# Optimization experiments

Measured on AMD Instinct MI355X. Metric: run time of the kernel, lower is better.

Reference implementation:

```python
import jax, jax.numpy as jnp
import numpy as np


def setup_inputs() -> dict:
    key = jax.random.key(0)
    k1, k2 = jax.random.split(key)
    n = 12000
    dataset = jax.random.normal(k1, (n,), dtype=jnp.float32)
    weights = jax.random.uniform(k2, (n,), dtype=jnp.float32)
    return {"dataset": dataset, "weights": weights}


def reference(dataset, weights):
    # normalize weights (update_weights)
    w = weights / jnp.sum(weights)
    neff = jnp.sum(w) ** 2 / jnp.sum(w ** 2)
    # Silverman's factor (torch.std is unbiased -> ddof=1; torch.quantile is linear interp)
    std_dev = jnp.std(dataset, ddof=1)
    iqr = jnp.quantile(dataset, 0.75) - jnp.quantile(dataset, 0.25)
    sigma_hat = jnp.minimum(std_dev, iqr / 1.34)
    h = 0.9 * sigma_hat * neff ** (-0.2)
    inv_norm = 1.0 / (h * jnp.sqrt(2.0 * jnp.pi))
    # pairwise Gaussian kernel matrix: [n, n]
    diff = (dataset[:, None] - dataset[None, :]) / h
    kernel = jnp.exp(-0.5 * diff * diff) * inv_norm
    pdf = kernel @ w  # [n]
    return jnp.log(pdf + 1e-10)
```

## Files before the change

### kernel.cpp

```cpp
#include <hip/hip_runtime.h>
#include <math.h>


#define BLK 256
#define NB 2048
#define NPART 12
#define CUT 4.0f

#if defined(__has_builtin)
#if __has_builtin(__builtin_amdgcn_exp2f)
#define EXP2(x) __builtin_amdgcn_exp2f(x)
#endif
#endif
#ifndef EXP2
#define EXP2(x) exp2f(x)
#endif

__global__ __launch_bounds__(1024) void kM(const float* __restrict__ d,
                                           const float* __restrict__ w,
                                           float4* __restrict__ statP,
                                           float2* __restrict__ mmP,
                                           int n) {
    __shared__ float4 sstat[16];
    __shared__ float2 smm[16];
    const int t = threadIdx.x, lane = t & 63, wid = t >> 6;
    const int i = blockIdx.x * 1024 + t;
    const bool ok = (i < n);
    float dv = ok ? d[i] : 0.f;
    float wv = ok ? w[i] : 0.f;
    float mn = ok ? dv : __int_as_float(0x7f800000);
    float mx = ok ? dv : __int_as_float(0xff800000);
    float s1 = wv, s2 = wv * wv, sd = dv, sd2 = dv * dv;
    for (int off = 32; off > 0; off >>= 1) {
        s1 += __shfl_down(s1, off); s2 += __shfl_down(s2, off);
        sd += __shfl_down(sd, off); sd2 += __shfl_down(sd2, off);
        mn = fminf(mn, __shfl_down(mn, off));
        mx = fmaxf(mx, __shfl_down(mx, off));
    }
    if (lane == 0) { sstat[wid] = make_float4(s1, s2, sd, sd2); smm[wid] = make_float2(mn, mx); }
    __syncthreads();
    if (t == 0) {
        float4 a = sstat[0]; float2 m = smm[0];
        for (int q = 1; q < 16; ++q) {
            float4 b = sstat[q];
            a.x += b.x; a.y += b.y; a.z += b.z; a.w += b.w;
            m.x = fminf(m.x, smm[q].x); m.y = fmaxf(m.y, smm[q].y);
        }
        statP[blockIdx.x] = a;
        mmP[blockIdx.x] = m;
    }
}

__global__ __launch_bounds__(1024) void kA(const float* __restrict__ d,
                                           const float* __restrict__ w,
                                           const float2* __restrict__ mmP,
                                           int* __restrict__ partH,
                                           float* __restrict__ partW,
                                           float* __restrict__ partWE,
                                           int n) {
    __shared__ int   hl[NB];
    __shared__ float wl[NB];
    __shared__ float wel[NB];
    const int t = threadIdx.x, blk = blockIdx.x;

    hl[t] = 0; hl[t + 1024] = 0;
    wl[t] = 0.f; wl[t + 1024] = 0.f;
    wel[t] = 0.f; wel[t + 1024] = 0.f;

    float lo = __int_as_float(0x7f800000), hi = __int_as_float(0xff800000);
    #pragma unroll
    for (int p = 0; p < NPART; ++p) {
        float2 m = mmP[p];
        lo = fminf(lo, m.x); hi = fmaxf(hi, m.y);
    }
    const float range = hi - lo;
    const float scale = (range > 0.f) ? (float)NB / range : 0.f;
    __syncthreads();

    const int i = blk * 1024 + t;
    if (i < n) {
        float dv = d[i], wv = w[i];
        int b = (int)((dv - lo) * scale);
        b = b < NB ? b : NB - 1;
        atomicAdd(&hl[b], 1);
        atomicAdd(&wl[b], wv);
        atomicAdd(&wel[b], wv * dv);
    }
    __syncthreads();

    partH [blk * NB + t] = hl[t];  partH [blk * NB + t + 1024] = hl[t + 1024];
    partW [blk * NB + t] = wl[t];  partW [blk * NB + t + 1024] = wl[t + 1024];
    partWE[blk * NB + t] = wel[t]; partWE[blk * NB + t + 1024] = wel[t + 1024];
}

__global__ __launch_bounds__(1024) void kB(const float4* __restrict__ statP,
                                           const float2* __restrict__ mmP,
                                           const int* __restrict__ partH,
                                           const float* __restrict__ partW,
                                           const float* __restrict__ partWE,
                                           float* __restrict__ params,
                                           float2* __restrict__ sb,
                                           int n) {
    __shared__ int cum[NB];
    __shared__ float sW[NB];
    __shared__ float sWE[NB];
    __shared__ int wtot[17];
    __shared__ float qv[4];
    __shared__ int tbin[4], tprev[4];
    __shared__ float spar[8];
    const int t = threadIdx.x, lane = t & 63, wid = t >> 6;
    const int b0 = t, b1 = t + 1024;

    int h0 = 0, h1 = 0;
    float W0 = 0.f, W1 = 0.f, E0 = 0.f, E1 = 0.f;
    #pragma unroll
    for (int p = 0; p < NPART; ++p) {
        h0 += partH[p * NB + b0];  h1 += partH[p * NB + b1];
        W0 += partW[p * NB + b0];  W1 += partW[p * NB + b1];
        E0 += partWE[p * NB + b0]; E1 += partWE[p * NB + b1];
    }
    sW[b0] = W0; sW[b1] = W1; sWE[b0] = E0; sWE[b1] = E1;

    int v = h0;
    for (int off = 1; off < 64; off <<= 1) {
        int u = __shfl_up(v, off);
        if (lane >= off) v += u;
    }
    if (lane == 63) wtot[wid] = v;
    __syncthreads();
    if (t == 0) {
        int acc = 0;
        for (int q = 0; q < 16; ++q) { int tmp = wtot[q]; wtot[q] = acc; acc += tmp; }
        wtot[16] = acc;
    }
    __syncthreads();
    cum[b0] = v + wtot[wid];
    const int half1 = wtot[16];
    __syncthreads();
    v = h1;
    for (int off = 1; off < 64; off <<= 1) {
        int u = __shfl_up(v, off);
        if (lane >= off) v += u;
    }
    if (lane == 63) wtot[wid] = v;
    __syncthreads();
    if (t == 0) {
        int acc = 0;
        for (int q = 0; q < 16; ++q) { int tmp = wtot[q]; wtot[q] = acc; acc += tmp; }
    }
    __syncthreads();
    cum[b1] = v + wtot[wid] + half1;
    __syncthreads();

    float lo = __int_as_float(0x7f800000), hi = __int_as_float(0xff800000);
    #pragma unroll
    for (int p = 0; p < NPART; ++p) {
        float2 m = mmP[p];
        lo = fminf(lo, m.x); hi = fmaxf(hi, m.y);
    }
    const float range = hi - lo;
    const float scale = (range > 0.f) ? (float)NB / range : 0.f;
    const float binw = (scale > 0.f) ? 1.0f / scale : 0.f;

    const double p25 = 0.25 * (double)(n - 1);
    const double p75 = 0.75 * (double)(n - 1);
    const int l25 = (int)p25, l75 = (int)p75;
    const int u25 = (l25 + 1 < n) ? l25 + 1 : l25;
    const int u75 = (l75 + 1 < n) ? l75 + 1 : l75;
    const int targets[4] = {l25, u25, l75, u75};
    {
        int prev0 = b0 ? cum[b0 - 1] : 0;
        int prev1 = cum[b1 - 1];
        #pragma unroll
        for (int r = 0; r < 4; ++r) {
            int k = targets[r];
            if (prev0 <= k && k < cum[b0]) { tbin[r] = b0; tprev[r] = prev0; }
            if (prev1 <= k && k < cum[b1]) { tbin[r] = b1; tprev[r] = prev1; }
        }
    }
    __syncthreads();
    if (t == 0) {
        #pragma unroll
        for (int r = 0; r < 4; ++r) {
            int b = tbin[r];
            int cnt = cum[b] - tprev[r];
            float pos = (float)b + ((float)(targets[r] - tprev[r]) + 0.5f) / (float)cnt;
            qv[r] = lo + pos * binw;
        }
        double S1 = 0, S2 = 0, Sd = 0, Sd2 = 0;
        for (int p = 0; p < NPART; ++p) {
            float4 a = statP[p];
            S1 += a.x; S2 += a.y; Sd += a.z; Sd2 += a.w;
        }
        float neff = (float)(S1 * S1 / S2);
        float varf = (float)((Sd2 - Sd * Sd / (double)n) / ((double)n - 1.0));
        float sdev = sqrtf(varf);
        float f25 = (float)(p25 - (double)l25), f75 = (float)(p75 - (double)l75);
        float q25 = qv[0] + f25 * (qv[1] - qv[0]);
        float q75 = qv[2] + f75 * (qv[3] - qv[2]);
        float sig = fminf(sdev, (q75 - q25) * (1.0f / 1.34f));
        float h = 0.9f * sig * exp2f(-0.2f * log2f(neff));
        float rr = 0.84932180f / h;
        float wsc = 1.0f / (h * 2.50662827f * (float)S1);
        float delta = (scale > 0.f && rr > 0.f)
                      ? ceilf(CUT * scale / rr) + 2.0f : (float)NB;
        spar[0] = lo; spar[1] = scale; spar[2] = rr; spar[3] = wsc; spar[4] = delta;
        params[0] = lo; params[1] = scale; params[2] = rr; params[3] = wsc; params[4] = delta;
    }
    __syncthreads();
    const float rr = spar[2], wsc = spar[3];
    {
        float mu0 = (sW[b0] > 0.f) ? (sWE[b0] / sW[b0]) : 0.f;
        float mu1 = (sW[b1] > 0.f) ? (sWE[b1] / sW[b1]) : 0.f;
        sb[b0] = make_float2(mu0 * rr, sW[b0] * wsc);
        sb[b1] = make_float2(mu1 * rr, sW[b1] * wsc);
    }
}

__global__ __launch_bounds__(BLK) void k3(const float* __restrict__ d,
                                          const float* __restrict__ params,
                                          const float2* __restrict__ sbG,
                                          float* __restrict__ out, int n) {
    __shared__ float2 sb[NB];
    __shared__ float sred[BLK];
    const int t = threadIdx.x, lane = t & 63, wv = t >> 6;
    const float lo = params[0], scale = params[1], rr = params[2];
    const int delta = (int)params[4];

    for (int idx = t; idx < NB; idx += BLK) sb[idx] = sbG[idx];

    const int i = blockIdx.x * 64 + lane;
    const float di = (i < n) ? d[i] : 0.f;
    const float ei = di * rr;
    int bi = (int)((di - lo) * scale);
    bi = bi < NB ? bi : NB - 1; if (bi < 0) bi = 0;
    int b0 = bi - delta; if (b0 < 0) b0 = 0;
    int b1 = bi + delta; if (b1 > NB - 1) b1 = NB - 1;
    const int len = b1 - b0 + 1;
    const int q = (len + 3) >> 2;
    int s = b0 + wv * q;
    int e = s + q; if (e > b1 + 1) e = b1 + 1;

    __syncthreads();

    float acc0 = 0.f, acc1 = 0.f;
    int b = s;
    for (; b + 1 < e; b += 2) {
        float2 p0 = sb[b], p1 = sb[b + 1];
        float u0 = ei - p0.x, u1 = ei - p1.x;
        acc0 = fmaf(p0.y, EXP2(-(u0 * u0)), acc0);
        acc1 = fmaf(p1.y, EXP2(-(u1 * u1)), acc1);
    }
    if (b < e) {
        float2 p0 = sb[b];
        float u0 = ei - p0.x;
        acc0 = fmaf(p0.y, EXP2(-(u0 * u0)), acc0);
    }

    sred[wv * 64 + lane] = acc0 + acc1;
    __syncthreads();
    if (t < 64) {
        int ii = blockIdx.x * 64 + t;
        if (ii < n) {
            float p = sred[t] + sred[64 + t] + sred[128 + t] + sred[192 + t];
            out[ii] = logf(p + 1e-10f);
        }
    }
}

extern "C" void kernel_launch(void* const* d_in, const int* in_sizes, int n_in,
                              void* d_out, int out_size, void* d_ws, size_t ws_size,
                              hipStream_t stream) {
    const float* d = (const float*)d_in[0];
    const float* w = (const float*)d_in[1];
    float* out = (float*)d_out;
    const int n = in_sizes[0];

    const int nmax = ((n + 63) / 64) * 64;
    const int G3 = nmax / 64;

    float*  wsf    = (float*)d_ws;
    float4* statP  = (float4*)wsf;
    float2* mmP    = (float2*)(wsf + 48);
    float*  params = wsf + 48 + 24;
    float2* sb     = (float2*)(wsf + 48 + 24 + 16);
    int*    partH  = (int*)(wsf + 48 + 24 + 16 + 2 * NB);
    float*  partW  = wsf + 48 + 24 + 16 + 2 * NB + NPART * NB;
    float*  partWE = wsf + 48 + 24 + 16 + 2 * NB + 2 * NPART * NB;

    kM<<<NPART, 1024, 0, stream>>>(d, w, statP, mmP, n);
    kA<<<NPART, 1024, 0, stream>>>(d, w, mmP, partH, partW, partWE, n);
    kB<<<1, 1024, 0, stream>>>(statP, mmP, partH, partW, partWE, params, sb, n);
    k3<<<G3, BLK, 0, stream>>>(d, params, sb, out, n);
}
```

Measured before the change: 28.54 us.

## Merge histogram partials via global atomics and fold the finalize kernel into the KDE kernel

The single-block finalize kernel is removed. kA now merges its per-block histograms into one global histogram with atomics, and kM zeroes that histogram first. Every block of the KDE kernel then recomputes the prefix scan, the quantiles, the bandwidth and the bin tables redundantly in shared memory. This cuts one launch and its serial single-block stage, at the cost of redundant per-block work in k3 and contended global atomics. Zeroing covers 12*512 = 6144 floats, which matches the 3*2048 floats of the three global arrays.

```diff
diff --git a/kernel.cpp b/kernel.cpp
--- a/kernel.cpp
+++ b/kernel.cpp
@@ -20,10 +20,13 @@
                                            const float* __restrict__ w,
                                            float4* __restrict__ statP,
                                            float2* __restrict__ mmP,
+                                           float* __restrict__ gZero,
                                            int n) {
     __shared__ float4 sstat[16];
     __shared__ float2 smm[16];
     const int t = threadIdx.x, lane = t & 63, wid = t >> 6;
+    if (t < 512) gZero[blockIdx.x * 512 + t] = 0.f;
+
     const int i = blockIdx.x * 1024 + t;
     const bool ok = (i < n);
     float dv = ok ? d[i] : 0.f;
@@ -54,14 +57,14 @@
 __global__ __launch_bounds__(1024) void kA(const float* __restrict__ d,
                                            const float* __restrict__ w,
                                            const float2* __restrict__ mmP,
-                                           int* __restrict__ partH,
-                                           float* __restrict__ partW,
-                                           float* __restrict__ partWE,
+                                           int* __restrict__ gH,
+                                           float* __restrict__ gW,
+                                           float* __restrict__ gWE,
                                            int n) {
     __shared__ int   hl[NB];
     __shared__ float wl[NB];
     __shared__ float wel[NB];
-    const int t = threadIdx.x, blk = blockIdx.x;
+    const int t = threadIdx.x;
 
     hl[t] = 0; hl[t + 1024] = 0;
     wl[t] = 0.f; wl[t + 1024] = 0.f;
@@ -77,7 +80,7 @@
     const float scale = (range > 0.f) ? (float)NB / range : 0.f;
     __syncthreads();
 
-    const int i = blk * 1024 + t;
+    const int i = blockIdx.x * 1024 + t;
     if (i < n) {
         float dv = d[i], wv = w[i];
         int b = (int)((dv - lo) * scale);
@@ -88,79 +91,67 @@
     }
     __syncthreads();
 
-    partH [blk * NB + t] = hl[t];  partH [blk * NB + t + 1024] = hl[t + 1024];
-    partW [blk * NB + t] = wl[t];  partW [blk * NB + t + 1024] = wl[t + 1024];
-    partWE[blk * NB + t] = wel[t]; partWE[blk * NB + t + 1024] = wel[t + 1024];
-}
-
-__global__ __launch_bounds__(1024) void kB(const float4* __restrict__ statP,
-                                           const float2* __restrict__ mmP,
-                                           const int* __restrict__ partH,
-                                           const float* __restrict__ partW,
-                                           const float* __restrict__ partWE,
-                                           float* __restrict__ params,
-                                           float2* __restrict__ sb,
-                                           int n) {
+    #pragma unroll
+    for (int k = 0; k < 2; ++k) {
+        int b = t + k * 1024;
+        int hv = hl[b];
+        if (hv) {
+            atomicAdd(&gH[b], hv);
+            atomicAdd(&gW[b], wl[b]);
+            atomicAdd(&gWE[b], wel[b]);
+        }
+    }
+}
+
+__global__ __launch_bounds__(BLK) void k3(const float* __restrict__ d,
+                                          const float4* __restrict__ statP,
+                                          const float2* __restrict__ mmP,
+                                          const int* __restrict__ gH,
+                                          const float* __restrict__ gW,
+                                          const float* __restrict__ gWE,
+                                          float* __restrict__ out, int n) {
+    __shared__ float2 sb[NB];
     __shared__ int cum[NB];
-    __shared__ float sW[NB];
-    __shared__ float sWE[NB];
-    __shared__ int wtot[17];
-    __shared__ float qv[4];
+    __shared__ int woff[4];
     __shared__ int tbin[4], tprev[4];
-    __shared__ float spar[8];
-    const int t = threadIdx.x, lane = t & 63, wid = t >> 6;
-    const int b0 = t, b1 = t + 1024;
-
-    int h0 = 0, h1 = 0;
-    float W0 = 0.f, W1 = 0.f, E0 = 0.f, E1 = 0.f;
+    __shared__ float spar[4];
+    __shared__ float sred[BLK];
+    const int t = threadIdx.x, lane = t & 63, wv = t >> 6;
+
+    float lo = __int_as_float(0x7f800000), hi = __int_as_float(0xff800000);
     #pragma unroll
     for (int p = 0; p < NPART; ++p) {
-        h0 += partH[p * NB + b0];  h1 += partH[p * NB + b1];
-        W0 += partW[p * NB + b0];  W1 += partW[p * NB + b1];
-        E0 += partWE[p * NB + b0]; E1 += partWE[p * NB + b1];
-    }
-    sW[b0] = W0; sW[b1] = W1; sWE[b0] = E0; sWE[b1] = E1;
-
-    int v = h0;
+        float2 m = mmP[p];
+        lo = fminf(lo, m.x); hi = fmaxf(hi, m.y);
+    }
+    const float range = hi - lo;
+    const float scale = (range > 0.f) ? (float)NB / range : 0.f;
+    const float binw = (scale > 0.f) ? 1.0f / scale : 0.f;
+
+    const int base = t * 8;
+    int h8[8], pre[8];
+    int s = 0;
+    #pragma unroll
+    for (int k = 0; k < 8; ++k) {
+        int b = base + k;
+        h8[k] = gH[b];
+        sb[b] = make_float2(gWE[b], gW[b]);
+        s += h8[k];
+        pre[k] = s;
+    }
+    int v = s;
     for (int off = 1; off < 64; off <<= 1) {
         int u = __shfl_up(v, off);
         if (lane >= off) v += u;
     }
-    if (lane == 63) wtot[wid] = v;
-    __syncthreads();
-    if (t == 0) {
-        int acc = 0;
-        for (int q = 0; q < 16; ++q) { int tmp = wtot[q]; wtot[q] = acc; acc += tmp; }
-        wtot[16] = acc;
-    }
-    __syncthreads();
-    cum[b0] = v + wtot[wid];
-    const int half1 = wtot[16];
-    __syncthreads();
-    v = h1;
-    for (int off = 1; off < 64; off <<= 1) {
-        int u = __shfl_up(v, off);
-        if (lane >= off) v += u;
-    }
-    if (lane == 63) wtot[wid] = v;
-    __syncthreads();
-    if (t == 0) {
-        int acc = 0;
-        for (int q = 0; q < 16; ++q) { int tmp = wtot[q]; wtot[q] = acc; acc += tmp; }
-    }
-    __syncthreads();
-    cum[b1] = v + wtot[wid] + half1;
-    __syncthreads();
-
-    float lo = __int_as_float(0x7f800000), hi = __int_as_float(0xff800000);
-    #pragma unroll
-    for (int p = 0; p < NPART; ++p) {
-        float2 m = mmP[p];
-        lo = fminf(lo, m.x); hi = fmaxf(hi, m.y);
-    }
-    const float range = hi - lo;
-    const float scale = (range > 0.f) ? (float)NB / range : 0.f;
-    const float binw = (scale > 0.f) ? 1.0f / scale : 0.f;
+    if (lane == 63) woff[wv] = v;
+    __syncthreads();
+    int wexcl = 0;
+    #pragma unroll
+    for (int q = 0; q < 4; ++q) if (q < wv) wexcl += woff[q];
+    const int texcl = wexcl + (v - s);
+    #pragma unroll
+    for (int k = 0; k < 8; ++k) cum[base + k] = texcl + pre[k];
 
     const double p25 = 0.25 * (double)(n - 1);
     const double p75 = 0.75 * (double)(n - 1);
@@ -168,18 +159,18 @@
     const int u25 = (l25 + 1 < n) ? l25 + 1 : l25;
     const int u75 = (l75 + 1 < n) ? l75 + 1 : l75;
     const int targets[4] = {l25, u25, l75, u75};
-    {
-        int prev0 = b0 ? cum[b0 - 1] : 0;
-        int prev1 = cum[b1 - 1];
+    #pragma unroll
+    for (int k = 0; k < 8; ++k) {
+        int prev = texcl + (k ? pre[k - 1] : 0);
+        int incl = texcl + pre[k];
         #pragma unroll
-        for (int r = 0; r < 4; ++r) {
-            int k = targets[r];
-            if (prev0 <= k && k < cum[b0]) { tbin[r] = b0; tprev[r] = prev0; }
-            if (prev1 <= k && k < cum[b1]) { tbin[r] = b1; tprev[r] = prev1; }
-        }
-    }
-    __syncthreads();
+        for (int r = 0; r < 4; ++r)
+            if (prev <= targets[r] && targets[r] < incl) { tbin[r] = base + k; tprev[r] = prev; }
+    }
+    __syncthreads();
+
     if (t == 0) {
+        float qv[4];
         #pragma unroll
         for (int r = 0; r < 4; ++r) {
             int b = tbin[r];
@@ -199,35 +190,26 @@
         float q25 = qv[0] + f25 * (qv[1] - qv[0]);
         float q75 = qv[2] + f75 * (qv[3] - qv[2]);
         float sig = fminf(sdev, (q75 - q25) * (1.0f / 1.34f));
-        float h = 0.9f * sig * exp2f(-0.2f * log2f(neff));
-        float rr = 0.84932180f / h;
-        float wsc = 1.0f / (h * 2.50662827f * (float)S1);
+        float hb = 0.9f * sig * exp2f(-0.2f * log2f(neff));
+        float rr = 0.84932180f / hb;
+        float wsc = 1.0f / (hb * 2.50662827f * (float)S1);
         float delta = (scale > 0.f && rr > 0.f)
                       ? ceilf(CUT * scale / rr) + 2.0f : (float)NB;
-        spar[0] = lo; spar[1] = scale; spar[2] = rr; spar[3] = wsc; spar[4] = delta;
-        params[0] = lo; params[1] = scale; params[2] = rr; params[3] = wsc; params[4] = delta;
-    }
-    __syncthreads();
-    const float rr = spar[2], wsc = spar[3];
-    {
-        float mu0 = (sW[b0] > 0.f) ? (sWE[b0] / sW[b0]) : 0.f;
-        float mu1 = (sW[b1] > 0.f) ? (sWE[b1] / sW[b1]) : 0.f;
-        sb[b0] = make_float2(mu0 * rr, sW[b0] * wsc);
-        sb[b1] = make_float2(mu1 * rr, sW[b1] * wsc);
-    }
-}
-
-__global__ __launch_bounds__(BLK) void k3(const float* __restrict__ d,
-                                          const float* __restrict__ params,
-                                          const float2* __restrict__ sbG,
-                                          float* __restrict__ out, int n) {
-    __shared__ float2 sb[NB];
-    __shared__ float sred[BLK];
-    const int t = threadIdx.x, lane = t & 63, wv = t >> 6;
-    const float lo = params[0], scale = params[1], rr = params[2];
-    const int delta = (int)params[4];
-
-    for (int idx = t; idx < NB; idx += BLK) sb[idx] = sbG[idx];
+        spar[0] = rr; spar[1] = wsc; spar[2] = delta;
+    }
+    __syncthreads();
+    const float rr = spar[0], wsc = spar[1];
+    const int delta = (int)spar[2];
+
+    #pragma unroll
+    for (int k = 0; k < 8; ++k) {
+        int b = base + k;
+        float2 vr = sb[b];
+        float W = vr.y;
+        float mu = (W > 0.f) ? (vr.x / W) : 0.f;
+        sb[b] = make_float2(mu * rr, W * wsc);
+    }
+    __syncthreads();
 
     const int i = blockIdx.x * 64 + lane;
     const float di = (i < n) ? d[i] : 0.f;
@@ -238,20 +220,18 @@
     int b1 = bi + delta; if (b1 > NB - 1) b1 = NB - 1;
     const int len = b1 - b0 + 1;
     const int q = (len + 3) >> 2;
-    int s = b0 + wv * q;
-    int e = s + q; if (e > b1 + 1) e = b1 + 1;
-
-    __syncthreads();
+    int ws_ = b0 + wv * q;
+    int we_ = ws_ + q; if (we_ > b1 + 1) we_ = b1 + 1;
 
     float acc0 = 0.f, acc1 = 0.f;
-    int b = s;
-    for (; b + 1 < e; b += 2) {
+    int b = ws_;
+    for (; b + 1 < we_; b += 2) {
         float2 p0 = sb[b], p1 = sb[b + 1];
         float u0 = ei - p0.x, u1 = ei - p1.x;
         acc0 = fmaf(p0.y, EXP2(-(u0 * u0)), acc0);
         acc1 = fmaf(p1.y, EXP2(-(u1 * u1)), acc1);
     }
-    if (b < e) {
+    if (b < we_) {
         float2 p0 = sb[b];
         float u0 = ei - p0.x;
         acc0 = fmaf(p0.y, EXP2(-(u0 * u0)), acc0);
@@ -279,17 +259,15 @@
     const int nmax = ((n + 63) / 64) * 64;
     const int G3 = nmax / 64;
 
-    float*  wsf    = (float*)d_ws;
-    float4* statP  = (float4*)wsf;
-    float2* mmP    = (float2*)(wsf + 48);
-    float*  params = wsf + 48 + 24;
-    float2* sb     = (float2*)(wsf + 48 + 24 + 16);
-    int*    partH  = (int*)(wsf + 48 + 24 + 16 + 2 * NB);
-    float*  partW  = wsf + 48 + 24 + 16 + 2 * NB + NPART * NB;
-    float*  partWE = wsf + 48 + 24 + 16 + 2 * NB + 2 * NPART * NB;
-
-    kM<<<NPART, 1024, 0, stream>>>(d, w, statP, mmP, n);
-    kA<<<NPART, 1024, 0, stream>>>(d, w, mmP, partH, partW, partWE, n);
-    kB<<<1, 1024, 0, stream>>>(statP, mmP, partH, partW, partWE, params, sb, n);
-    k3<<<G3, BLK, 0, stream>>>(d, params, sb, out, n);
-}
+    float*  wsf   = (float*)d_ws;
+    float4* statP = (float4*)wsf;
+    float2* mmP   = (float2*)(wsf + 48);
+    float*  gZero = wsf + 80;
+    int*    gH    = (int*)(wsf + 80);
+    float*  gW    = wsf + 80 + NB;
+    float*  gWE   = wsf + 80 + 2 * NB;
+
+    kM<<<NPART, 1024, 0, stream>>>(d, w, statP, mmP, gZero, n);
+    kA<<<NPART, 1024, 0, stream>>>(d, w, mmP, gH, gW, gWE, n);
+    k3<<<G3, BLK, 0, stream>>>(d, statP, mmP, gH, gW, gWE, out, n);
+}
```

Measured after the change: 24.08 us. 1.19x faster.
